# Kernel optimization log

Measured on AMD Instinct MI355X. Metric: run time of the kernel, lower is better.

Reference implementation:

```python
import jax, jax.numpy as jnp
import numpy as np

B = 1024
IN_Q = 2048
IN_KV = 2048
NH = 16
D = 64
INNER = NH * D
TF = 4
NC = 2
EPS = 1e-5
SLOPE = 0.01  # LeakyReLU default negative slope


def setup_inputs() -> dict:
    key = jax.random.key(0)
    ks = jax.random.split(key, 8)
    s = 0.02
    return {
        "q_input": jax.random.normal(ks[0], (B, IN_Q), jnp.float32),
        "kv_input": jax.random.normal(ks[1], (B, IN_KV), jnp.float32),
        "Wq": jax.random.normal(ks[2], (INNER, IN_Q), jnp.float32) * s,
        "bq": jax.random.normal(ks[3], (INNER,), jnp.float32) * s,
        "Wkv": jax.random.normal(ks[4], (2 * INNER, IN_KV), jnp.float32) * s,
        "bkv": jax.random.normal(ks[5], (2 * INNER,), jnp.float32) * s,
        "bn_w": jnp.ones((TF,), jnp.float32),
        "bn_b": jnp.zeros((TF,), jnp.float32),
        "Wo": jax.random.normal(ks[6], (NC, TF), jnp.float32) * s,
        "bo": jax.random.normal(ks[7], (NC,), jnp.float32) * s,
    }


def reference(q_input, kv_input, Wq, bq, Wkv, bkv, bn_w, bn_b, Wo, bo):
    b = q_input.shape[0]
    # projections: [B, NH, D] and [B, NH, 2D]
    q = (q_input @ Wq.T + bq).reshape(b, NH, D)
    kv = (kv_input @ Wkv.T + bkv).reshape(b, NH, 2 * D)
    k, v = kv[..., :D], kv[..., D:]
    # sim[b,n] = k[b,n,:] . q[b,n,:]  (per-head scalar score)
    sim = jnp.einsum("bnd,bnd->bn", k, q)
    att = jax.nn.softmax(sim, axis=-1)  # softmax over heads
    # torch.matmul([B,NH], [B,NH,D]) broadcast -> out[i,j,:] = sum_n att[j,n] v[i,n,:]
    att_out = jnp.einsum("jn,ind->ijd", att, v)  # [B, B, D]
    flat = att_out.reshape(b, b * D)  # [B, B*D]
    # AdaptiveAvgPool1d to TF bins (L % TF == 0 -> exact reshape-mean)
    pooled = flat.reshape(b, TF, (b * D) // TF).mean(axis=-1)  # [B, TF]
    x = jnp.where(pooled >= 0, pooled, SLOPE * pooled)  # LeakyReLU
    # BatchNorm1d, train mode (batch stats, biased variance)
    mean = x.mean(axis=0)
    var = x.var(axis=0)
    x = (x - mean) * jax.lax.rsqrt(var + EPS) * bn_w + bn_b
    # dropout(p=0.0) is identity
    return x @ Wo.T + bo  # [B, NC]
```

## Files before the change

### kernel.cpp

```cpp
#include <hip/hip_runtime.h>
#include <hip/hip_bf16.h>

#define EPS 1e-5f
#define SLOPE 0.01f

typedef __attribute__((ext_vector_type(8))) short bfrag8;
typedef __attribute__((ext_vector_type(4))) float f32x4;

#define AS1 __attribute__((address_space(1)))
#define AS3 __attribute__((address_space(3)))

#define WS_SIM_OFF   0u
#define WS_S_OFF     65536u
#define WS_WVS_OFF   131072u
#define WS_BVS_OFF   262144u
#define WS_OUT_OFF   262208u
#define WS_AIMG_OFF  8650816u
#define WS_BIMG_OFF  25428032u

__device__ __forceinline__ unsigned short f2bf(float f) {
    union { float f; unsigned int u; } x; x.f = f;
    unsigned int r = (x.u + 0x7FFFu + ((x.u >> 16) & 1u)) >> 16;
    return (unsigned short)r;
}
__device__ __forceinline__ uint4 pack8(const float4& a, const float4& b) {
    uint4 r;
    r.x = (unsigned)f2bf(a.x) | ((unsigned)f2bf(a.y) << 16);
    r.y = (unsigned)f2bf(a.z) | ((unsigned)f2bf(a.w) << 16);
    r.z = (unsigned)f2bf(b.x) | ((unsigned)f2bf(b.y) << 16);
    r.w = (unsigned)f2bf(b.z) | ((unsigned)f2bf(b.w) << 16);
    return r;
}

#define PREP_A    524288
#define PREP_B2   (PREP_A + 524288)
#define PREP_WVSE (PREP_B2 + 32768)
#define PREP_END  (PREP_WVSE + 16)

__global__ __launch_bounds__(256) void prep_kernel(
        const float* __restrict__ qin, const float* __restrict__ kvin,
        const float* __restrict__ Wq, const float* __restrict__ Wkv,
        const float* __restrict__ bkv, unsigned char* __restrict__ ws) {
    int gid = blockIdx.x * 256 + threadIdx.x;
    if (gid < PREP_A) {
        int p  = gid & 511;
        int kt = (gid >> 9) & 31;
        int mt = (gid >> 14) & 15;
        int s2 = gid >> 18;
        int rit = p >> 3;
        int gk = (p & 7) ^ (rit & 7);
        int row = mt * 64 + rit;
        int k = kt * 64 + gk * 8;
        const float* src = (s2 ? kvin : qin) + (size_t)row * 2048 + k;
        float4 v0 = *(const float4*)src;
        float4 v1 = *(const float4*)(src + 4);
        *(uint4*)(ws + WS_AIMG_OFF + (size_t)gid * 16) = pack8(v0, v1);
    } else if (gid < PREP_B2) {
        int g2 = gid - PREP_A;
        int p  = g2 & 511;
        int kt = (g2 >> 9) & 31;
        int nt = g2 >> 14;
        int cit = p >> 3;
        int gk = (p & 7) ^ (cit & 7);
        int col = nt * 64 + cit;
        int k = kt * 64 + gk * 8;
        const float* wrow;
        if (col < 1024) wrow = Wq + (size_t)col * 2048;
        else {
            int c2 = col - 1024;
            wrow = Wkv + (size_t)(((c2 >> 6) << 7) + (c2 & 63)) * 2048;
        }
        float4 v0 = *(const float4*)(wrow + k);
        float4 v1 = *(const float4*)(wrow + k + 4);
        *(uint4*)(ws + WS_BIMG_OFF + (size_t)g2 * 16) = pack8(v0, v1);
    } else if (gid < PREP_WVSE) {
        int g2 = gid - PREP_B2;
        int n = g2 >> 11, c = g2 & 2047;
        const float* base = Wkv + (size_t)(n * 128 + 64) * 2048 + c;
        float s = 0.f;
        #pragma unroll 8
        for (int d = 0; d < 64; ++d) s += base[(size_t)d * 2048];
        ((float*)(ws + WS_WVS_OFF))[c * 16 + n] = s;
    } else if (gid < PREP_END) {
        int n = gid - PREP_WVSE;
        float b = 0.f;
        #pragma unroll
        for (int d = 0; d < 64; ++d) b += bkv[n * 128 + 64 + d];
        ((float*)(ws + WS_BVS_OFF))[n] = b;
    }
}

__global__ __launch_bounds__(256, 2) void gemm_qk_kernel(unsigned char* __restrict__ ws) {
    __shared__ alignas(16) unsigned short LA[3][4096];
    __shared__ alignas(16) unsigned short LB[3][4096];

    const int t = threadIdx.x;
    const int w = t >> 6, l = t & 63;
    const int nt = blockIdx.x, mt = blockIdx.y;
    const int wr = w >> 1, wc = w & 1;
    const int lrow = l & 15, lhi = l >> 4;

    const unsigned char* aBase = ws + WS_AIMG_OFF
        + (size_t)((nt >= 16) ? 4194304u : 0u) + (size_t)mt * 262144u;
    const unsigned char* bBase = ws + WS_BIMG_OFF + (size_t)nt * 262144u;
    float* Out = (float*)(ws + WS_OUT_OFF);

    int offA[2][2], offB[2][2];
    #pragma unroll
    for (int ks = 0; ks < 2; ++ks)
        #pragma unroll
        for (int i = 0; i < 2; ++i) {
            int rA = wr * 32 + i * 16 + lrow;
            int rB = wc * 32 + i * 16 + lrow;
            offA[ks][i] = rA * 128 + (((ks * 4 + lhi) ^ (rA & 7)) << 4);
            offB[ks][i] = rB * 128 + (((ks * 4 + lhi) ^ (rB & 7)) << 4);
        }

    f32x4 acc00 = (f32x4)0.f, acc01 = (f32x4)0.f, acc10 = (f32x4)0.f, acc11 = (f32x4)0.f;

#define STAGE(kt_, buf_) do {                                                        \
    const unsigned char* _as = aBase + (size_t)(kt_) * 8192;                         \
    const unsigned char* _bs = bBase + (size_t)(kt_) * 8192;                         \
    unsigned char* _ad = ((unsigned char*)&LA[0][0]) + (size_t)(buf_) * 8192;        \
    unsigned char* _bd = ((unsigned char*)&LB[0][0]) + (size_t)(buf_) * 8192;        \
    _Pragma("unroll")                                                                \
    for (int _j = 0; _j < 2; ++_j) {                                                 \
        int _p = _j * 256 + t;                                                       \
        __builtin_amdgcn_global_load_lds(                                            \
            (const AS1 unsigned int*)(const void*)(_as + _p * 16),                   \
            (AS3 unsigned int*)(void*)(_ad + _p * 16), 16, 0, 0);                    \
        __builtin_amdgcn_global_load_lds(                                            \
            (const AS1 unsigned int*)(const void*)(_bs + _p * 16),                   \
            (AS3 unsigned int*)(void*)(_bd + _p * 16), 16, 0, 0);                    \
    } } while (0)

    STAGE(0, 0);
    STAGE(1, 1);
    asm volatile("s_waitcnt vmcnt(4)" ::: "memory");
    __builtin_amdgcn_sched_barrier(0);
    __builtin_amdgcn_s_barrier();
    __builtin_amdgcn_sched_barrier(0);

    int cur = 0, nxt = 2;
    for (int kt = 0; kt < 32; ++kt) {
        const char* la = (const char*)&LA[0][0] + cur * 8192;
        const char* lb = (const char*)&LB[0][0] + cur * 8192;
        bfrag8 fa00 = *(const bfrag8*)(la + offA[0][0]);
        bfrag8 fa01 = *(const bfrag8*)(la + offA[0][1]);
        bfrag8 fa10 = *(const bfrag8*)(la + offA[1][0]);
        bfrag8 fa11 = *(const bfrag8*)(la + offA[1][1]);
        bfrag8 fb00 = *(const bfrag8*)(lb + offB[0][0]);
        bfrag8 fb01 = *(const bfrag8*)(lb + offB[0][1]);
        bfrag8 fb10 = *(const bfrag8*)(lb + offB[1][0]);
        bfrag8 fb11 = *(const bfrag8*)(lb + offB[1][1]);
        acc00 = __builtin_amdgcn_mfma_f32_16x16x32_bf16(fa00, fb00, acc00, 0, 0, 0);
        acc01 = __builtin_amdgcn_mfma_f32_16x16x32_bf16(fa00, fb01, acc01, 0, 0, 0);
        acc10 = __builtin_amdgcn_mfma_f32_16x16x32_bf16(fa01, fb00, acc10, 0, 0, 0);
        acc11 = __builtin_amdgcn_mfma_f32_16x16x32_bf16(fa01, fb01, acc11, 0, 0, 0);
        acc00 = __builtin_amdgcn_mfma_f32_16x16x32_bf16(fa10, fb10, acc00, 0, 0, 0);
        acc01 = __builtin_amdgcn_mfma_f32_16x16x32_bf16(fa10, fb11, acc01, 0, 0, 0);
        acc10 = __builtin_amdgcn_mfma_f32_16x16x32_bf16(fa11, fb10, acc10, 0, 0, 0);
        acc11 = __builtin_amdgcn_mfma_f32_16x16x32_bf16(fa11, fb11, acc11, 0, 0, 0);
        if (kt < 30) {
            STAGE(kt + 2, nxt);
            asm volatile("s_waitcnt vmcnt(4)" ::: "memory");
        } else {
            asm volatile("s_waitcnt vmcnt(0)" ::: "memory");
        }
        __builtin_amdgcn_sched_barrier(0);
        __builtin_amdgcn_s_barrier();
        __builtin_amdgcn_sched_barrier(0);
        cur = (cur == 2) ? 0 : cur + 1;
        nxt = (nxt == 2) ? 0 : nxt + 1;
    }
#undef STAGE

    f32x4 acc[2][2] = {{acc00, acc01}, {acc10, acc11}};
    #pragma unroll
    for (int mi = 0; mi < 2; ++mi)
        #pragma unroll
        for (int ni = 0; ni < 2; ++ni) {
            int col = nt * 64 + wc * 32 + ni * 16 + lrow;
            #pragma unroll
            for (int r = 0; r < 4; ++r) {
                int row = mt * 64 + wr * 32 + mi * 16 + lhi * 4 + r;
                Out[(size_t)row * 2048 + col] = acc[mi][ni][r];
            }
        }
}

__global__ __launch_bounds__(256) void sim_s_kernel(
        const float* __restrict__ bq, const float* __restrict__ bkv,
        const float* __restrict__ kvin, unsigned char* __restrict__ ws) {
    int b = blockIdx.x, t = threadIdx.x;
    int w = t >> 6, l = t & 63;
    {
        const float* orow = (const float*)(ws + WS_OUT_OFF) + (size_t)b * 2048;
        float* sim = (float*)(ws + WS_SIM_OFF);
        #pragma unroll
        for (int hh = 0; hh < 4; ++hh) {
            int h = w * 4 + hh;
            float qv = orow[h * 64 + l]        + bq[h * 64 + l];
            float kv = orow[1024 + h * 64 + l] + bkv[h * 128 + l];
            float p = qv * kv;
            p += __shfl_xor(p, 1);  p += __shfl_xor(p, 2);
            p += __shfl_xor(p, 4);  p += __shfl_xor(p, 8);
            p += __shfl_xor(p, 16); p += __shfl_xor(p, 32);
            if (l == 0) sim[b * 16 + h] = p;
        }
    }
    __shared__ float SW[4][16];
    int n = t & 15, g = t >> 4;
    const float* kvrow = kvin + (size_t)b * 2048;
    const float* wv = (const float*)(ws + WS_WVS_OFF);
    float p = 0.f;
    #pragma unroll 4
    for (int tt = 0; tt < 128; ++tt) {
        int c = g + (tt << 4);
        p = fmaf(kvrow[c], wv[c * 16 + n], p);
    }
    p += __shfl_xor(p, 16);
    p += __shfl_xor(p, 32);
    if (l < 16) SW[w][n] = p;
    __syncthreads();
    if (t < 16) {
        float sv = SW[0][t] + SW[1][t] + SW[2][t] + SW[3][t]
                 + ((const float*)(ws + WS_BVS_OFF))[t];
        ((float*)(ws + WS_S_OFF))[b * 16 + t] = sv;
    }
}

__global__ __launch_bounds__(1024) void final_kernel(
        const float* __restrict__ bn_w, const float* __restrict__ bn_b,
        const float* __restrict__ Wo, const float* __restrict__ bo,
        const unsigned char* __restrict__ ws, float* __restrict__ out) {
    int t = threadIdx.x;
    int w = t >> 6;
    int l = t & 63;
    __shared__ float Aw[16][16];
    __shared__ float Af[4][16];
    __shared__ float SWs[16][8];
    __shared__ float FS[8];
    __shared__ float sc[4], sh[4];

    float a16[16];
    {
        const float* srow = (const float*)(ws + WS_SIM_OFF) + (size_t)t * 16;
        float4 v0 = *(const float4*)(srow + 0);
        float4 v1 = *(const float4*)(srow + 4);
        float4 v2 = *(const float4*)(srow + 8);
        float4 v3 = *(const float4*)(srow + 12);
        a16[0]=v0.x; a16[1]=v0.y; a16[2]=v0.z; a16[3]=v0.w;
        a16[4]=v1.x; a16[5]=v1.y; a16[6]=v1.z; a16[7]=v1.w;
        a16[8]=v2.x; a16[9]=v2.y; a16[10]=v2.z; a16[11]=v2.w;
        a16[12]=v3.x; a16[13]=v3.y; a16[14]=v3.z; a16[15]=v3.w;
        float m = a16[0];
        #pragma unroll
        for (int n = 1; n < 16; ++n) m = fmaxf(m, a16[n]);
        float den = 0.f;
        #pragma unroll
        for (int n = 0; n < 16; ++n) { a16[n] = expf(a16[n] - m); den += a16[n]; }
        float inv = 1.f / den;
        #pragma unroll
        for (int n = 0; n < 16; ++n) a16[n] *= inv;
    }
    #pragma unroll
    for (int n = 0; n < 16; ++n) {
        float p = a16[n];
        p += __shfl_xor(p, 1);  p += __shfl_xor(p, 2);
        p += __shfl_xor(p, 4);  p += __shfl_xor(p, 8);
        p += __shfl_xor(p, 16); p += __shfl_xor(p, 32);
        a16[n] = p;
    }
    if (l == 0) {
        #pragma unroll
        for (int n = 0; n < 16; ++n) Aw[w][n] = a16[n];
    }
    __syncthreads();
    if (t < 64) {
        int f = t >> 4, n = t & 15;
        Af[f][n] = Aw[4*f][n] + Aw[4*f+1][n] + Aw[4*f+2][n] + Aw[4*f+3][n];
    }
    __syncthreads();

    float sv[16];
    {
        const float* srow = (const float*)(ws + WS_S_OFF) + (size_t)t * 16;
        float4 v0 = *(const float4*)(srow + 0);
        float4 v1 = *(const float4*)(srow + 4);
        float4 v2 = *(const float4*)(srow + 8);
        float4 v3 = *(const float4*)(srow + 12);
        sv[0]=v0.x; sv[1]=v0.y; sv[2]=v0.z; sv[3]=v0.w;
        sv[4]=v1.x; sv[5]=v1.y; sv[6]=v1.z; sv[7]=v1.w;
        sv[8]=v2.x; sv[9]=v2.y; sv[10]=v2.z; sv[11]=v2.w;
        sv[12]=v3.x; sv[13]=v3.y; sv[14]=v3.z; sv[15]=v3.w;
    }
    float x[4];
    #pragma unroll
    for (int f = 0; f < 4; ++f) {
        float p = 0.f;
        #pragma unroll
        for (int n = 0; n < 16; ++n) p = fmaf(Af[f][n], sv[n], p);
        p *= (1.f / 16384.f);
        x[f] = (p >= 0.f) ? p : SLOPE * p;
    }

    float st[8];
    #pragma unroll
    for (int f = 0; f < 4; ++f) { st[f] = x[f]; st[4 + f] = x[f] * x[f]; }
    #pragma unroll
    for (int j = 0; j < 8; ++j) {
        float p = st[j];
        p += __shfl_xor(p, 1);  p += __shfl_xor(p, 2);
        p += __shfl_xor(p, 4);  p += __shfl_xor(p, 8);
        p += __shfl_xor(p, 16); p += __shfl_xor(p, 32);
        st[j] = p;
    }
    if (l == 0) {
        #pragma unroll
        for (int j = 0; j < 8; ++j) SWs[w][j] = st[j];
    }
    __syncthreads();
    if (t < 8) {
        float p = 0.f;
        #pragma unroll
        for (int ww = 0; ww < 16; ++ww) p += SWs[ww][t];
        FS[t] = p;
    }
    __syncthreads();
    if (t < 4) {
        float mean = FS[t] * (1.f / 1024.f);
        float var  = FS[4 + t] * (1.f / 1024.f) - mean * mean;
        float s = bn_w[t] / sqrtf(var + EPS);
        sc[t] = s;
        sh[t] = bn_b[t] - mean * s;
    }
    __syncthreads();

    float o0 = bo[0], o1 = bo[1];
    #pragma unroll
    for (int f = 0; f < 4; ++f) {
        float xh = x[f] * sc[f] + sh[f];
        o0 = fmaf(xh, Wo[f], o0);
        o1 = fmaf(xh, Wo[4 + f], o1);
    }
    *(float2*)(out + (size_t)t * 2) = make_float2(o0, o1);
}

extern "C" void kernel_launch(void* const* d_in, const int* in_sizes, int n_in,
                              void* d_out, int out_size, void* d_ws, size_t ws_size,
                              hipStream_t stream) {
    const float* q_input  = (const float*)d_in[0];
    const float* kv_input = (const float*)d_in[1];
    const float* Wq   = (const float*)d_in[2];
    const float* bq   = (const float*)d_in[3];
    const float* Wkv  = (const float*)d_in[4];
    const float* bkv  = (const float*)d_in[5];
    const float* bn_w = (const float*)d_in[6];
    const float* bn_b = (const float*)d_in[7];
    const float* Wo   = (const float*)d_in[8];
    const float* bo   = (const float*)d_in[9];
    float* out = (float*)d_out;
    unsigned char* ws = (unsigned char*)d_ws;

    hipLaunchKernelGGL(prep_kernel, dim3((PREP_END + 255) / 256), dim3(256), 0, stream,
                       q_input, kv_input, Wq, Wkv, bkv, ws);
    hipLaunchKernelGGL(gemm_qk_kernel, dim3(32, 16), dim3(256), 0, stream, ws);
    hipLaunchKernelGGL(sim_s_kernel, dim3(1024), dim3(256), 0, stream,
                       bq, bkv, kv_input, ws);
    hipLaunchKernelGGL(final_kernel, dim3(1), dim3(1024), 0, stream,
                       bn_w, bn_b, Wo, bo, ws, out);
}
```

Measured before the change: 62.94 us.

## Enlarge GEMM tiles to 128x128 with split-K over two partial outputs

The projection GEMM moves from 64x64 tiles and 512 blocks to 128x128 tiles split along K into two halves, giving 256 blocks. Each writes a partial result to its own buffer, and the sim kernel adds the two partials. The prep layout changes to match the larger tiles, and the pipeline becomes four-stage with 16 accumulators per wave. The aim is better operand reuse per LDS load and fewer global loads, at the cost of extra partial-sum traffic, 128KB of LDS per block and lower occupancy.

New measurement: 66.25 us. 5.3% more time.

```diff
diff --git a/kernel.cpp b/kernel.cpp
--- a/kernel.cpp
+++ b/kernel.cpp
@@ -14,8 +14,9 @@
 #define WS_S_OFF     65536u
 #define WS_WVS_OFF   131072u
 #define WS_BVS_OFF   262144u
-#define WS_OUT_OFF   262208u
-#define WS_AIMG_OFF  8650816u
+#define WS_OUT0_OFF  262208u
+#define WS_OUT1_OFF  8650816u
+#define WS_AIMG_OFF  17039424u
 #define WS_BIMG_OFF  25428032u
 
 __device__ __forceinline__ unsigned short f2bf(float f) {
@@ -43,27 +44,27 @@
         const float* __restrict__ bkv, unsigned char* __restrict__ ws) {
     int gid = blockIdx.x * 256 + threadIdx.x;
     if (gid < PREP_A) {
-        int p  = gid & 511;
-        int kt = (gid >> 9) & 31;
-        int mt = (gid >> 14) & 15;
-        int s2 = gid >> 18;
+        int p   = gid & 1023;
+        int ktg = (gid >> 10) & 31;
+        int mt  = (gid >> 15) & 7;
+        int s2  = gid >> 18;
         int rit = p >> 3;
-        int gk = (p & 7) ^ (rit & 7);
-        int row = mt * 64 + rit;
-        int k = kt * 64 + gk * 8;
+        int gk  = (p & 7) ^ (rit & 7);
+        int row = mt * 128 + rit;
+        int k   = ktg * 64 + gk * 8;
         const float* src = (s2 ? kvin : qin) + (size_t)row * 2048 + k;
         float4 v0 = *(const float4*)src;
         float4 v1 = *(const float4*)(src + 4);
         *(uint4*)(ws + WS_AIMG_OFF + (size_t)gid * 16) = pack8(v0, v1);
     } else if (gid < PREP_B2) {
-        int g2 = gid - PREP_A;
-        int p  = g2 & 511;
-        int kt = (g2 >> 9) & 31;
-        int nt = g2 >> 14;
+        int g2  = gid - PREP_A;
+        int p   = g2 & 1023;
+        int ktg = (g2 >> 10) & 31;
+        int nt  = g2 >> 15;
         int cit = p >> 3;
-        int gk = (p & 7) ^ (cit & 7);
-        int col = nt * 64 + cit;
-        int k = kt * 64 + gk * 8;
+        int gk  = (p & 7) ^ (cit & 7);
+        int col = nt * 128 + cit;
+        int k   = ktg * 64 + gk * 8;
         const float* wrow;
         if (col < 1024) wrow = Wq + (size_t)col * 2048;
         else {
@@ -90,41 +91,47 @@
     }
 }
 
-__global__ __launch_bounds__(256, 2) void gemm_qk_kernel(unsigned char* __restrict__ ws) {
-    __shared__ alignas(16) unsigned short LA[3][4096];
-    __shared__ alignas(16) unsigned short LB[3][4096];
+__global__ __launch_bounds__(256) void gemm_qk_kernel(unsigned char* __restrict__ ws) {
+    __shared__ alignas(16) unsigned short LA[4][8192];
+    __shared__ alignas(16) unsigned short LB[4][8192];
 
     const int t = threadIdx.x;
     const int w = t >> 6, l = t & 63;
-    const int nt = blockIdx.x, mt = blockIdx.y;
+    const int nt = blockIdx.x, mt = blockIdx.y, kz = blockIdx.z;
     const int wr = w >> 1, wc = w & 1;
     const int lrow = l & 15, lhi = l >> 4;
 
     const unsigned char* aBase = ws + WS_AIMG_OFF
-        + (size_t)((nt >= 16) ? 4194304u : 0u) + (size_t)mt * 262144u;
-    const unsigned char* bBase = ws + WS_BIMG_OFF + (size_t)nt * 262144u;
-    float* Out = (float*)(ws + WS_OUT_OFF);
-
-    int offA[2][2], offB[2][2];
+        + (size_t)((nt >= 8) ? 4194304u : 0u) + (size_t)mt * 524288u
+        + (size_t)kz * 262144u;
+    const unsigned char* bBase = ws + WS_BIMG_OFF
+        + (size_t)nt * 524288u + (size_t)kz * 262144u;
+    float* Out = (float*)(ws + (kz ? WS_OUT1_OFF : WS_OUT0_OFF));
+
+    int offA[2][4], offB[2][4];
     #pragma unroll
     for (int ks = 0; ks < 2; ++ks)
         #pragma unroll
-        for (int i = 0; i < 2; ++i) {
-            int rA = wr * 32 + i * 16 + lrow;
-            int rB = wc * 32 + i * 16 + lrow;
+        for (int i = 0; i < 4; ++i) {
+            int rA = wr * 64 + i * 16 + lrow;
+            int rB = wc * 64 + i * 16 + lrow;
             offA[ks][i] = rA * 128 + (((ks * 4 + lhi) ^ (rA & 7)) << 4);
             offB[ks][i] = rB * 128 + (((ks * 4 + lhi) ^ (rB & 7)) << 4);
         }
 
-    f32x4 acc00 = (f32x4)0.f, acc01 = (f32x4)0.f, acc10 = (f32x4)0.f, acc11 = (f32x4)0.f;
+    f32x4 acc[4][4];
+    #pragma unroll
+    for (int mi = 0; mi < 4; ++mi)
+        #pragma unroll
+        for (int ni = 0; ni < 4; ++ni) acc[mi][ni] = (f32x4)0.f;
 
 #define STAGE(kt_, buf_) do {                                                        \
-    const unsigned char* _as = aBase + (size_t)(kt_) * 8192;                         \
-    const unsigned char* _bs = bBase + (size_t)(kt_) * 8192;                         \
-    unsigned char* _ad = ((unsigned char*)&LA[0][0]) + (size_t)(buf_) * 8192;        \
-    unsigned char* _bd = ((unsigned char*)&LB[0][0]) + (size_t)(buf_) * 8192;        \
+    const unsigned char* _as = aBase + (size_t)(kt_) * 16384;                        \
+    const unsigned char* _bs = bBase + (size_t)(kt_) * 16384;                        \
+    unsigned char* _ad = ((unsigned char*)&LA[0][0]) + (size_t)(buf_) * 16384;       \
+    unsigned char* _bd = ((unsigned char*)&LB[0][0]) + (size_t)(buf_) * 16384;       \
     _Pragma("unroll")                                                                \
-    for (int _j = 0; _j < 2; ++_j) {                                                 \
+    for (int _j = 0; _j < 4; ++_j) {                                                 \
         int _p = _j * 256 + t;                                                       \
         __builtin_amdgcn_global_load_lds(                                            \
             (const AS1 unsigned int*)(const void*)(_as + _p * 16),                   \
@@ -136,54 +143,49 @@
 
     STAGE(0, 0);
     STAGE(1, 1);
-    asm volatile("s_waitcnt vmcnt(4)" ::: "memory");
+    STAGE(2, 2);
+    asm volatile("s_waitcnt vmcnt(16)" ::: "memory");
     __builtin_amdgcn_sched_barrier(0);
     __builtin_amdgcn_s_barrier();
     __builtin_amdgcn_sched_barrier(0);
 
-    int cur = 0, nxt = 2;
-    for (int kt = 0; kt < 32; ++kt) {
-        const char* la = (const char*)&LA[0][0] + cur * 8192;
-        const char* lb = (const char*)&LB[0][0] + cur * 8192;
-        bfrag8 fa00 = *(const bfrag8*)(la + offA[0][0]);
-        bfrag8 fa01 = *(const bfrag8*)(la + offA[0][1]);
-        bfrag8 fa10 = *(const bfrag8*)(la + offA[1][0]);
-        bfrag8 fa11 = *(const bfrag8*)(la + offA[1][1]);
-        bfrag8 fb00 = *(const bfrag8*)(lb + offB[0][0]);
-        bfrag8 fb01 = *(const bfrag8*)(lb + offB[0][1]);
-        bfrag8 fb10 = *(const bfrag8*)(lb + offB[1][0]);
-        bfrag8 fb11 = *(const bfrag8*)(lb + offB[1][1]);
-        acc00 = __builtin_amdgcn_mfma_f32_16x16x32_bf16(fa00, fb00, acc00, 0, 0, 0);
-        acc01 = __builtin_amdgcn_mfma_f32_16x16x32_bf16(fa00, fb01, acc01, 0, 0, 0);
-        acc10 = __builtin_amdgcn_mfma_f32_16x16x32_bf16(fa01, fb00, acc10, 0, 0, 0);
-        acc11 = __builtin_amdgcn_mfma_f32_16x16x32_bf16(fa01, fb01, acc11, 0, 0, 0);
-        acc00 = __builtin_amdgcn_mfma_f32_16x16x32_bf16(fa10, fb10, acc00, 0, 0, 0);
-        acc01 = __builtin_amdgcn_mfma_f32_16x16x32_bf16(fa10, fb11, acc01, 0, 0, 0);
-        acc10 = __builtin_amdgcn_mfma_f32_16x16x32_bf16(fa11, fb10, acc10, 0, 0, 0);
-        acc11 = __builtin_amdgcn_mfma_f32_16x16x32_bf16(fa11, fb11, acc11, 0, 0, 0);
-        if (kt < 30) {
-            STAGE(kt + 2, nxt);
-            asm volatile("s_waitcnt vmcnt(4)" ::: "memory");
-        } else {
-            asm volatile("s_waitcnt vmcnt(0)" ::: "memory");
-        }
+    for (int kt = 0; kt < 16; ++kt) {
+        const int cur = kt & 3;
+        if (kt <= 12) STAGE(kt + 3, (kt + 3) & 3);
+        const char* la = (const char*)&LA[0][0] + (size_t)cur * 16384;
+        const char* lb = (const char*)&LB[0][0] + (size_t)cur * 16384;
+        #pragma unroll
+        for (int ks = 0; ks < 2; ++ks) {
+            bfrag8 fa[4], fb[4];
+            #pragma unroll
+            for (int i = 0; i < 4; ++i) {
+                fa[i] = *(const bfrag8*)(la + offA[ks][i]);
+                fb[i] = *(const bfrag8*)(lb + offB[ks][i]);
+            }
+            #pragma unroll
+            for (int mi = 0; mi < 4; ++mi)
+                #pragma unroll
+                for (int ni = 0; ni < 4; ++ni)
+                    acc[mi][ni] = __builtin_amdgcn_mfma_f32_16x16x32_bf16(
+                        fa[mi], fb[ni], acc[mi][ni], 0, 0, 0);
+        }
+        if (kt <= 12)      asm volatile("s_waitcnt vmcnt(16)" ::: "memory");
+        else if (kt == 13) asm volatile("s_waitcnt vmcnt(8)"  ::: "memory");
+        else               asm volatile("s_waitcnt vmcnt(0)"  ::: "memory");
         __builtin_amdgcn_sched_barrier(0);
         __builtin_amdgcn_s_barrier();
         __builtin_amdgcn_sched_barrier(0);
-        cur = (cur == 2) ? 0 : cur + 1;
-        nxt = (nxt == 2) ? 0 : nxt + 1;
     }
 #undef STAGE
 
-    f32x4 acc[2][2] = {{acc00, acc01}, {acc10, acc11}};
-    #pragma unroll
-    for (int mi = 0; mi < 2; ++mi)
-        #pragma unroll
-        for (int ni = 0; ni < 2; ++ni) {
-            int col = nt * 64 + wc * 32 + ni * 16 + lrow;
+    #pragma unroll
+    for (int mi = 0; mi < 4; ++mi)
+        #pragma unroll
+        for (int ni = 0; ni < 4; ++ni) {
+            int col = nt * 128 + wc * 64 + ni * 16 + lrow;
             #pragma unroll
             for (int r = 0; r < 4; ++r) {
-                int row = mt * 64 + wr * 32 + mi * 16 + lhi * 4 + r;
+                int row = mt * 128 + wr * 64 + mi * 16 + lhi * 4 + r;
                 Out[(size_t)row * 2048 + col] = acc[mi][ni][r];
             }
         }
@@ -195,13 +197,14 @@
     int b = blockIdx.x, t = threadIdx.x;
     int w = t >> 6, l = t & 63;
     {
-        const float* orow = (const float*)(ws + WS_OUT_OFF) + (size_t)b * 2048;
+        const float* o0 = (const float*)(ws + WS_OUT0_OFF) + (size_t)b * 2048;
+        const float* o1 = (const float*)(ws + WS_OUT1_OFF) + (size_t)b * 2048;
         float* sim = (float*)(ws + WS_SIM_OFF);
         #pragma unroll
         for (int hh = 0; hh < 4; ++hh) {
             int h = w * 4 + hh;
-            float qv = orow[h * 64 + l]        + bq[h * 64 + l];
-            float kv = orow[1024 + h * 64 + l] + bkv[h * 128 + l];
+            float qv = o0[h * 64 + l]        + o1[h * 64 + l]        + bq[h * 64 + l];
+            float kv = o0[1024 + h * 64 + l] + o1[1024 + h * 64 + l] + bkv[h * 128 + l];
             float p = qv * kv;
             p += __shfl_xor(p, 1);  p += __shfl_xor(p, 2);
             p += __shfl_xor(p, 4);  p += __shfl_xor(p, 8);
@@ -365,7 +368,7 @@
 
     hipLaunchKernelGGL(prep_kernel, dim3((PREP_END + 255) / 256), dim3(256), 0, stream,
                        q_input, kv_input, Wq, Wkv, bkv, ws);
-    hipLaunchKernelGGL(gemm_qk_kernel, dim3(32, 16), dim3(256), 0, stream, ws);
+    hipLaunchKernelGGL(gemm_qk_kernel, dim3(16, 8, 2), dim3(256), 0, stream, ws);
     hipLaunchKernelGGL(sim_s_kernel, dim3(1024), dim3(256), 0, stream,
                        bq, bkv, kv_input, ws);
     hipLaunchKernelGGL(final_kernel, dim3(1), dim3(1024), 0, stream,
```

## Convert activations to bf16 inside GEMM and read B fragments directly from global

Applied to the files above, without the earlier changes.

The prep kernel no longer pre-converts q/kv activations into a swizzled bf16 image. The GEMM now loads fp32 activations, converts them in registers with v_cvt_pk_bf16_f32, and writes them to a double-buffered LDS tile. Weights are pre-packed in MFMA fragment order so each wave reads its B fragments straight from global memory without LDS staging. This removes a full round trip of the activation image through memory and halves LDS use, at the cost of register-staged loads and uncached-in-LDS B reads whose latency may be less hidden.

Result: slower. 68.86 us (+9.4%).

```diff
diff --git a/kernel.cpp b/kernel.cpp
--- a/kernel.cpp
+++ b/kernel.cpp
@@ -6,17 +6,13 @@
 
 typedef __attribute__((ext_vector_type(8))) short bfrag8;
 typedef __attribute__((ext_vector_type(4))) float f32x4;
-
-#define AS1 __attribute__((address_space(1)))
-#define AS3 __attribute__((address_space(3)))
 
 #define WS_SIM_OFF   0u
 #define WS_S_OFF     65536u
 #define WS_WVS_OFF   131072u
 #define WS_BVS_OFF   262144u
 #define WS_OUT_OFF   262208u
-#define WS_AIMG_OFF  8650816u
-#define WS_BIMG_OFF  25428032u
+#define WS_BIMG_OFF  8650816u
 
 __device__ __forceinline__ unsigned short f2bf(float f) {
     union { float f; unsigned int u; } x; x.f = f;
@@ -31,39 +27,29 @@
     r.w = (unsigned)f2bf(b.z) | ((unsigned)f2bf(b.w) << 16);
     return r;
 }
-
-#define PREP_A    524288
-#define PREP_B2   (PREP_A + 524288)
+__device__ __forceinline__ unsigned cvtpk(float lo, float hi) {
+    unsigned r;
+    asm("v_cvt_pk_bf16_f32 %0, %1, %2" : "=v"(r) : "v"(lo), "v"(hi));
+    return r;
+}
+
+#define PREP_B2   524288
 #define PREP_WVSE (PREP_B2 + 32768)
 #define PREP_END  (PREP_WVSE + 16)
 
 __global__ __launch_bounds__(256) void prep_kernel(
-        const float* __restrict__ qin, const float* __restrict__ kvin,
         const float* __restrict__ Wq, const float* __restrict__ Wkv,
         const float* __restrict__ bkv, unsigned char* __restrict__ ws) {
     int gid = blockIdx.x * 256 + threadIdx.x;
-    if (gid < PREP_A) {
-        int p  = gid & 511;
-        int kt = (gid >> 9) & 31;
-        int mt = (gid >> 14) & 15;
-        int s2 = gid >> 18;
-        int rit = p >> 3;
-        int gk = (p & 7) ^ (rit & 7);
-        int row = mt * 64 + rit;
-        int k = kt * 64 + gk * 8;
-        const float* src = (s2 ? kvin : qin) + (size_t)row * 2048 + k;
-        float4 v0 = *(const float4*)src;
-        float4 v1 = *(const float4*)(src + 4);
-        *(uint4*)(ws + WS_AIMG_OFF + (size_t)gid * 16) = pack8(v0, v1);
-    } else if (gid < PREP_B2) {
-        int g2 = gid - PREP_A;
-        int p  = g2 & 511;
-        int kt = (g2 >> 9) & 31;
-        int nt = g2 >> 14;
-        int cit = p >> 3;
-        int gk = (p & 7) ^ (cit & 7);
-        int col = nt * 64 + cit;
-        int k = kt * 64 + gk * 8;
+    if (gid < PREP_B2) {
+        int l   = gid & 63;
+        int ni  = (gid >> 6) & 1;
+        int ks  = (gid >> 7) & 1;
+        int kt  = (gid >> 8) & 31;
+        int wcg = (gid >> 13) & 1;
+        int nt  = gid >> 14;
+        int col = nt * 64 + wcg * 32 + ni * 16 + (l & 15);
+        int k   = kt * 64 + ks * 32 + (l >> 4) * 8;
         const float* wrow;
         if (col < 1024) wrow = Wq + (size_t)col * 2048;
         else {
@@ -72,7 +58,7 @@
         }
         float4 v0 = *(const float4*)(wrow + k);
         float4 v1 = *(const float4*)(wrow + k + 4);
-        *(uint4*)(ws + WS_BIMG_OFF + (size_t)g2 * 16) = pack8(v0, v1);
+        *(uint4*)(ws + WS_BIMG_OFF + (size_t)gid * 16) = pack8(v0, v1);
     } else if (gid < PREP_WVSE) {
         int g2 = gid - PREP_B2;
         int n = g2 >> 11, c = g2 & 2047;
@@ -90,90 +76,101 @@
     }
 }
 
-__global__ __launch_bounds__(256, 2) void gemm_qk_kernel(unsigned char* __restrict__ ws) {
-    __shared__ alignas(16) unsigned short LA[3][4096];
-    __shared__ alignas(16) unsigned short LB[3][4096];
+__global__ __launch_bounds__(256) void gemm_qk_kernel(
+        const float* __restrict__ qin, const float* __restrict__ kvin,
+        unsigned char* __restrict__ ws) {
+    __shared__ alignas(16) unsigned short LA[2][4096];
 
     const int t = threadIdx.x;
     const int w = t >> 6, l = t & 63;
     const int nt = blockIdx.x, mt = blockIdx.y;
     const int wr = w >> 1, wc = w & 1;
     const int lrow = l & 15, lhi = l >> 4;
-
-    const unsigned char* aBase = ws + WS_AIMG_OFF
-        + (size_t)((nt >= 16) ? 4194304u : 0u) + (size_t)mt * 262144u;
-    const unsigned char* bBase = ws + WS_BIMG_OFF + (size_t)nt * 262144u;
+    const int m0 = mt * 64;
+
+    const int arow = t >> 2, aq4 = t & 3;
+    const int gk0 = aq4 * 2, gk1 = gk0 + 1;
+    const float* aSrc = ((nt >= 16) ? kvin : qin) + (size_t)(m0 + arow) * 2048;
+    const int adst0 = arow * 128 + ((gk0 ^ (arow & 7)) << 4);
+    const int adst1 = arow * 128 + ((gk1 ^ (arow & 7)) << 4);
+    unsigned char* lds = (unsigned char*)&LA[0][0];
+
+    const unsigned char* bP = ws + WS_BIMG_OFF
+        + (size_t)(nt * 2 + wc) * 131072 + (size_t)l * 16;
+
     float* Out = (float*)(ws + WS_OUT_OFF);
 
-    int offA[2][2], offB[2][2];
+    int offA[2][2];
     #pragma unroll
     for (int ks = 0; ks < 2; ++ks)
         #pragma unroll
         for (int i = 0; i < 2; ++i) {
-            int rA = wr * 32 + i * 16 + lrow;
-            int rB = wc * 32 + i * 16 + lrow;
-            offA[ks][i] = rA * 128 + (((ks * 4 + lhi) ^ (rA & 7)) << 4);
-            offB[ks][i] = rB * 128 + (((ks * 4 + lhi) ^ (rB & 7)) << 4);
+            int r = wr * 32 + i * 16 + lrow;
+            offA[ks][i] = r * 128 + (((ks * 4 + lhi) ^ (r & 7)) << 4);
         }
 
     f32x4 acc00 = (f32x4)0.f, acc01 = (f32x4)0.f, acc10 = (f32x4)0.f, acc11 = (f32x4)0.f;
 
-#define STAGE(kt_, buf_) do {                                                        \
-    const unsigned char* _as = aBase + (size_t)(kt_) * 8192;                         \
-    const unsigned char* _bs = bBase + (size_t)(kt_) * 8192;                         \
-    unsigned char* _ad = ((unsigned char*)&LA[0][0]) + (size_t)(buf_) * 8192;        \
-    unsigned char* _bd = ((unsigned char*)&LB[0][0]) + (size_t)(buf_) * 8192;        \
-    _Pragma("unroll")                                                                \
-    for (int _j = 0; _j < 2; ++_j) {                                                 \
-        int _p = _j * 256 + t;                                                       \
-        __builtin_amdgcn_global_load_lds(                                            \
-            (const AS1 unsigned int*)(const void*)(_as + _p * 16),                   \
-            (AS3 unsigned int*)(void*)(_ad + _p * 16), 16, 0, 0);                    \
-        __builtin_amdgcn_global_load_lds(                                            \
-            (const AS1 unsigned int*)(const void*)(_bs + _p * 16),                   \
-            (AS3 unsigned int*)(void*)(_bd + _p * 16), 16, 0, 0);                    \
+#define LOAD_A(kt_, S) do {                                                   \
+    S[0] = *(const float4*)(aSrc + (kt_) * 64 + gk0 * 8);                     \
+    S[1] = *(const float4*)(aSrc + (kt_) * 64 + gk0 * 8 + 4);                 \
+    S[2] = *(const float4*)(aSrc + (kt_) * 64 + gk1 * 8);                     \
+    S[3] = *(const float4*)(aSrc + (kt_) * 64 + gk1 * 8 + 4); } while (0)
+
+#define WRITE_A(S, buf_) do {                                                 \
+    uint4 _u0, _u1;                                                           \
+    _u0.x = cvtpk(S[0].x, S[0].y); _u0.y = cvtpk(S[0].z, S[0].w);             \
+    _u0.z = cvtpk(S[1].x, S[1].y); _u0.w = cvtpk(S[1].z, S[1].w);             \
+    _u1.x = cvtpk(S[2].x, S[2].y); _u1.y = cvtpk(S[2].z, S[2].w);             \
+    _u1.z = cvtpk(S[3].x, S[3].y); _u1.w = cvtpk(S[3].z, S[3].w);             \
+    *(uint4*)(lds + (buf_) * 8192 + adst0) = _u0;                             \
+    *(uint4*)(lds + (buf_) * 8192 + adst1) = _u1; } while (0)
+
+#define BARRIER() do {                                                        \
+    asm volatile("s_waitcnt lgkmcnt(0)" ::: "memory");                        \
+    __builtin_amdgcn_sched_barrier(0);                                        \
+    __builtin_amdgcn_s_barrier();                                             \
+    __builtin_amdgcn_sched_barrier(0); } while (0)
+
+#define COMPUTE(kt_, buf_) do {                                               \
+    const char* _la = (const char*)lds + (buf_) * 8192;                       \
+    const unsigned char* _bp = bP + (size_t)(kt_) * 4096;                     \
+    _Pragma("unroll")                                                         \
+    for (int _ks = 0; _ks < 2; ++_ks) {                                       \
+        bfrag8 _fa0 = *(const bfrag8*)(_la + offA[_ks][0]);                   \
+        bfrag8 _fa1 = *(const bfrag8*)(_la + offA[_ks][1]);                   \
+        bfrag8 _fb0 = *(const bfrag8*)(_bp + _ks * 2048);                     \
+        bfrag8 _fb1 = *(const bfrag8*)(_bp + _ks * 2048 + 1024);              \
+        acc00 = __builtin_amdgcn_mfma_f32_16x16x32_bf16(_fa0, _fb0, acc00, 0, 0, 0); \
+        acc01 = __builtin_amdgcn_mfma_f32_16x16x32_bf16(_fa0, _fb1, acc01, 0, 0, 0); \
+        acc10 = __builtin_amdgcn_mfma_f32_16x16x32_bf16(_fa1, _fb0, acc10, 0, 0, 0); \
+        acc11 = __builtin_amdgcn_mfma_f32_16x16x32_bf16(_fa1, _fb1, acc11, 0, 0, 0); \
     } } while (0)
 
-    STAGE(0, 0);
-    STAGE(1, 1);
-    asm volatile("s_waitcnt vmcnt(4)" ::: "memory");
-    __builtin_amdgcn_sched_barrier(0);
-    __builtin_amdgcn_s_barrier();
-    __builtin_amdgcn_sched_barrier(0);
-
-    int cur = 0, nxt = 2;
-    for (int kt = 0; kt < 32; ++kt) {
-        const char* la = (const char*)&LA[0][0] + cur * 8192;
-        const char* lb = (const char*)&LB[0][0] + cur * 8192;
-        bfrag8 fa00 = *(const bfrag8*)(la + offA[0][0]);
-        bfrag8 fa01 = *(const bfrag8*)(la + offA[0][1]);
-        bfrag8 fa10 = *(const bfrag8*)(la + offA[1][0]);
-        bfrag8 fa11 = *(const bfrag8*)(la + offA[1][1]);
-        bfrag8 fb00 = *(const bfrag8*)(lb + offB[0][0]);
-        bfrag8 fb01 = *(const bfrag8*)(lb + offB[0][1]);
-        bfrag8 fb10 = *(const bfrag8*)(lb + offB[1][0]);
-        bfrag8 fb11 = *(const bfrag8*)(lb + offB[1][1]);
-        acc00 = __builtin_amdgcn_mfma_f32_16x16x32_bf16(fa00, fb00, acc00, 0, 0, 0);
-        acc01 = __builtin_amdgcn_mfma_f32_16x16x32_bf16(fa00, fb01, acc01, 0, 0, 0);
-        acc10 = __builtin_amdgcn_mfma_f32_16x16x32_bf16(fa01, fb00, acc10, 0, 0, 0);
-        acc11 = __builtin_amdgcn_mfma_f32_16x16x32_bf16(fa01, fb01, acc11, 0, 0, 0);
-        acc00 = __builtin_amdgcn_mfma_f32_16x16x32_bf16(fa10, fb10, acc00, 0, 0, 0);
-        acc01 = __builtin_amdgcn_mfma_f32_16x16x32_bf16(fa10, fb11, acc01, 0, 0, 0);
-        acc10 = __builtin_amdgcn_mfma_f32_16x16x32_bf16(fa11, fb10, acc10, 0, 0, 0);
-        acc11 = __builtin_amdgcn_mfma_f32_16x16x32_bf16(fa11, fb11, acc11, 0, 0, 0);
-        if (kt < 30) {
-            STAGE(kt + 2, nxt);
-            asm volatile("s_waitcnt vmcnt(4)" ::: "memory");
-        } else {
-            asm volatile("s_waitcnt vmcnt(0)" ::: "memory");
-        }
-        __builtin_amdgcn_sched_barrier(0);
-        __builtin_amdgcn_s_barrier();
-        __builtin_amdgcn_sched_barrier(0);
-        cur = (cur == 2) ? 0 : cur + 1;
-        nxt = (nxt == 2) ? 0 : nxt + 1;
-    }
-#undef STAGE
+    float4 E[4], O[4];
+
+    LOAD_A(0, E);
+    WRITE_A(E, 0);
+    LOAD_A(1, O);
+    BARRIER();
+
+    for (int j = 0; j < 16; ++j) {
+        const int kt = 2 * j;
+        if (j < 15) LOAD_A(kt + 2, E);
+        COMPUTE(kt, 0);
+        WRITE_A(O, 1);
+        BARRIER();
+        if (j < 15) LOAD_A(kt + 3, O);
+        COMPUTE(kt + 1, 1);
+        if (j < 15) {
+            WRITE_A(E, 0);
+            BARRIER();
+        }
+    }
+#undef LOAD_A
+#undef WRITE_A
+#undef BARRIER
+#undef COMPUTE
 
     f32x4 acc[2][2] = {{acc00, acc01}, {acc10, acc11}};
     #pragma unroll
@@ -183,7 +180,7 @@
             int col = nt * 64 + wc * 32 + ni * 16 + lrow;
             #pragma unroll
             for (int r = 0; r < 4; ++r) {
-                int row = mt * 64 + wr * 32 + mi * 16 + lhi * 4 + r;
+                int row = m0 + wr * 32 + mi * 16 + lhi * 4 + r;
                 Out[(size_t)row * 2048 + col] = acc[mi][ni][r];
             }
         }
@@ -364,8 +361,9 @@
     unsigned char* ws = (unsigned char*)d_ws;
 
     hipLaunchKernelGGL(prep_kernel, dim3((PREP_END + 255) / 256), dim3(256), 0, stream,
-                       q_input, kv_input, Wq, Wkv, bkv, ws);
-    hipLaunchKernelGGL(gemm_qk_kernel, dim3(32, 16), dim3(256), 0, stream, ws);
+                       Wq, Wkv, bkv, ws);
+    hipLaunchKernelGGL(gemm_qk_kernel, dim3(32, 16), dim3(256), 0, stream,
+                       q_input, kv_input, ws);
     hipLaunchKernelGGL(sim_s_kernel, dim3(1024), dim3(256), 0, stream,
                        bq, bkv, kv_input, ws);
     hipLaunchKernelGGL(final_kernel, dim3(1), dim3(1024), 0, stream,
```

## Fuse per-head q·k score into projection GEMM epilogue with atomic accumulation

Applied to the files above, without the earlier changes.

Reorganizes the B-weight image so each GEMM block computes matching 32-column halves of the Q and K projections for one head. The q and k tiles are combined in the epilogue via shared memory, reduced with shuffles, and atomically added into the sim buffer, which prep now zeroes. This removes the 8 MB fp32 projection output write and its re-read in the follow-up kernel. In exchange each block loads three A/B tiles per k-step instead of two, uses more LDS, and the sim values are summed with float atomics, so their order is nondeterministic.

New measurement: 60.56 us. 1.04x faster.

```diff
diff --git a/kernel.cpp b/kernel.cpp
--- a/kernel.cpp
+++ b/kernel.cpp
@@ -14,9 +14,8 @@
 #define WS_S_OFF     65536u
 #define WS_WVS_OFF   131072u
 #define WS_BVS_OFF   262144u
-#define WS_OUT_OFF   262208u
-#define WS_AIMG_OFF  8650816u
-#define WS_BIMG_OFF  25428032u
+#define WS_AIMG_OFF  262208u
+#define WS_BIMG_OFF  8650816u
 
 __device__ __forceinline__ unsigned short f2bf(float f) {
     union { float f; unsigned int u; } x; x.f = f;
@@ -35,7 +34,8 @@
 #define PREP_A    524288
 #define PREP_B2   (PREP_A + 524288)
 #define PREP_WVSE (PREP_B2 + 32768)
-#define PREP_END  (PREP_WVSE + 16)
+#define PREP_SIMZ (PREP_WVSE + 16384)
+#define PREP_END  (PREP_SIMZ + 16)
 
 __global__ __launch_bounds__(256) void prep_kernel(
         const float* __restrict__ qin, const float* __restrict__ kvin,
@@ -59,17 +59,14 @@
         int g2 = gid - PREP_A;
         int p  = g2 & 511;
         int kt = (g2 >> 9) & 31;
-        int nt = g2 >> 14;
+        int dh = (g2 >> 14) & 1;
+        int h  = g2 >> 15;
         int cit = p >> 3;
         int gk = (p & 7) ^ (cit & 7);
-        int col = nt * 64 + cit;
         int k = kt * 64 + gk * 8;
         const float* wrow;
-        if (col < 1024) wrow = Wq + (size_t)col * 2048;
-        else {
-            int c2 = col - 1024;
-            wrow = Wkv + (size_t)(((c2 >> 6) << 7) + (c2 & 63)) * 2048;
-        }
+        if (cit < 32) wrow = Wq  + (size_t)(h * 64 + dh * 32 + cit) * 2048;
+        else          wrow = Wkv + (size_t)(h * 128 + dh * 32 + (cit - 32)) * 2048;
         float4 v0 = *(const float4*)(wrow + k);
         float4 v1 = *(const float4*)(wrow + k + 4);
         *(uint4*)(ws + WS_BIMG_OFF + (size_t)g2 * 16) = pack8(v0, v1);
@@ -81,8 +78,10 @@
         #pragma unroll 8
         for (int d = 0; d < 64; ++d) s += base[(size_t)d * 2048];
         ((float*)(ws + WS_WVS_OFF))[c * 16 + n] = s;
+    } else if (gid < PREP_SIMZ) {
+        ((float*)(ws + WS_SIM_OFF))[gid - PREP_WVSE] = 0.f;
     } else if (gid < PREP_END) {
-        int n = gid - PREP_WVSE;
+        int n = gid - PREP_SIMZ;
         float b = 0.f;
         #pragma unroll
         for (int d = 0; d < 64; ++d) b += bkv[n * 128 + 64 + d];
@@ -90,80 +89,86 @@
     }
 }
 
-__global__ __launch_bounds__(256, 2) void gemm_qk_kernel(unsigned char* __restrict__ ws) {
-    __shared__ alignas(16) unsigned short LA[3][4096];
+__global__ __launch_bounds__(256, 2) void gemm_sim_kernel(unsigned char* __restrict__ ws,
+        const float* __restrict__ bq, const float* __restrict__ bkv) {
+    __shared__ alignas(16) unsigned short LAq[3][4096];
+    __shared__ alignas(16) unsigned short LAkv[3][4096];
     __shared__ alignas(16) unsigned short LB[3][4096];
 
     const int t = threadIdx.x;
     const int w = t >> 6, l = t & 63;
-    const int nt = blockIdx.x, mt = blockIdx.y;
-    const int wr = w >> 1, wc = w & 1;
+    const int hd = blockIdx.x, mt = blockIdx.y;
+    const int h = hd >> 1, dh = hd & 1;
+    const int qk = w >> 1, wr = w & 1;
     const int lrow = l & 15, lhi = l >> 4;
-
-    const unsigned char* aBase = ws + WS_AIMG_OFF
-        + (size_t)((nt >= 16) ? 4194304u : 0u) + (size_t)mt * 262144u;
-    const unsigned char* bBase = ws + WS_BIMG_OFF + (size_t)nt * 262144u;
-    float* Out = (float*)(ws + WS_OUT_OFF);
+    const int m0 = mt * 64;
+
+    const unsigned char* aqBase = ws + WS_AIMG_OFF + (size_t)mt * 262144u;
+    const unsigned char* akBase = aqBase + 4194304u;
+    const unsigned char* bBase  = ws + WS_BIMG_OFF + (size_t)hd * 262144u;
+    float* sim = (float*)(ws + WS_SIM_OFF);
 
     int offA[2][2], offB[2][2];
     #pragma unroll
     for (int ks = 0; ks < 2; ++ks)
         #pragma unroll
         for (int i = 0; i < 2; ++i) {
-            int rA = wr * 32 + i * 16 + lrow;
-            int rB = wc * 32 + i * 16 + lrow;
-            offA[ks][i] = rA * 128 + (((ks * 4 + lhi) ^ (rA & 7)) << 4);
-            offB[ks][i] = rB * 128 + (((ks * 4 + lhi) ^ (rB & 7)) << 4);
+            int r = wr * 32 + i * 16 + lrow;
+            int c = qk * 32 + i * 16 + lrow;
+            offA[ks][i] = r * 128 + (((ks * 4 + lhi) ^ (r & 7)) << 4);
+            offB[ks][i] = c * 128 + (((ks * 4 + lhi) ^ (c & 7)) << 4);
         }
 
     f32x4 acc00 = (f32x4)0.f, acc01 = (f32x4)0.f, acc10 = (f32x4)0.f, acc11 = (f32x4)0.f;
 
 #define STAGE(kt_, buf_) do {                                                        \
-    const unsigned char* _as = aBase + (size_t)(kt_) * 8192;                         \
-    const unsigned char* _bs = bBase + (size_t)(kt_) * 8192;                         \
-    unsigned char* _ad = ((unsigned char*)&LA[0][0]) + (size_t)(buf_) * 8192;        \
-    unsigned char* _bd = ((unsigned char*)&LB[0][0]) + (size_t)(buf_) * 8192;        \
+    const unsigned char* _aq = aqBase + (size_t)(kt_) * 8192;                        \
+    const unsigned char* _ak = akBase + (size_t)(kt_) * 8192;                        \
+    const unsigned char* _b  = bBase  + (size_t)(kt_) * 8192;                        \
+    unsigned char* _dq = ((unsigned char*)&LAq[0][0])  + (size_t)(buf_) * 8192;      \
+    unsigned char* _dk = ((unsigned char*)&LAkv[0][0]) + (size_t)(buf_) * 8192;      \
+    unsigned char* _db = ((unsigned char*)&LB[0][0])   + (size_t)(buf_) * 8192;      \
     _Pragma("unroll")                                                                \
     for (int _j = 0; _j < 2; ++_j) {                                                 \
         int _p = _j * 256 + t;                                                       \
         __builtin_amdgcn_global_load_lds(                                            \
-            (const AS1 unsigned int*)(const void*)(_as + _p * 16),                   \
-            (AS3 unsigned int*)(void*)(_ad + _p * 16), 16, 0, 0);                    \
+            (const AS1 unsigned int*)(const void*)(_aq + _p * 16),                   \
+            (AS3 unsigned int*)(void*)(_dq + _p * 16), 16, 0, 0);                    \
         __builtin_amdgcn_global_load_lds(                                            \
-            (const AS1 unsigned int*)(const void*)(_bs + _p * 16),                   \
-            (AS3 unsigned int*)(void*)(_bd + _p * 16), 16, 0, 0);                    \
+            (const AS1 unsigned int*)(const void*)(_ak + _p * 16),                   \
+            (AS3 unsigned int*)(void*)(_dk + _p * 16), 16, 0, 0);                    \
+        __builtin_amdgcn_global_load_lds(                                            \
+            (const AS1 unsigned int*)(const void*)(_b + _p * 16),                    \
+            (AS3 unsigned int*)(void*)(_db + _p * 16), 16, 0, 0);                    \
     } } while (0)
 
     STAGE(0, 0);
     STAGE(1, 1);
-    asm volatile("s_waitcnt vmcnt(4)" ::: "memory");
+    asm volatile("s_waitcnt vmcnt(6)" ::: "memory");
     __builtin_amdgcn_sched_barrier(0);
     __builtin_amdgcn_s_barrier();
     __builtin_amdgcn_sched_barrier(0);
 
     int cur = 0, nxt = 2;
     for (int kt = 0; kt < 32; ++kt) {
-        const char* la = (const char*)&LA[0][0] + cur * 8192;
-        const char* lb = (const char*)&LB[0][0] + cur * 8192;
-        bfrag8 fa00 = *(const bfrag8*)(la + offA[0][0]);
-        bfrag8 fa01 = *(const bfrag8*)(la + offA[0][1]);
-        bfrag8 fa10 = *(const bfrag8*)(la + offA[1][0]);
-        bfrag8 fa11 = *(const bfrag8*)(la + offA[1][1]);
-        bfrag8 fb00 = *(const bfrag8*)(lb + offB[0][0]);
-        bfrag8 fb01 = *(const bfrag8*)(lb + offB[0][1]);
-        bfrag8 fb10 = *(const bfrag8*)(lb + offB[1][0]);
-        bfrag8 fb11 = *(const bfrag8*)(lb + offB[1][1]);
-        acc00 = __builtin_amdgcn_mfma_f32_16x16x32_bf16(fa00, fb00, acc00, 0, 0, 0);
-        acc01 = __builtin_amdgcn_mfma_f32_16x16x32_bf16(fa00, fb01, acc01, 0, 0, 0);
-        acc10 = __builtin_amdgcn_mfma_f32_16x16x32_bf16(fa01, fb00, acc10, 0, 0, 0);
-        acc11 = __builtin_amdgcn_mfma_f32_16x16x32_bf16(fa01, fb01, acc11, 0, 0, 0);
-        acc00 = __builtin_amdgcn_mfma_f32_16x16x32_bf16(fa10, fb10, acc00, 0, 0, 0);
-        acc01 = __builtin_amdgcn_mfma_f32_16x16x32_bf16(fa10, fb11, acc01, 0, 0, 0);
-        acc10 = __builtin_amdgcn_mfma_f32_16x16x32_bf16(fa11, fb10, acc10, 0, 0, 0);
-        acc11 = __builtin_amdgcn_mfma_f32_16x16x32_bf16(fa11, fb11, acc11, 0, 0, 0);
+        {
+            const char* Ab = (const char*)(qk ? &LAkv[0][0] : &LAq[0][0]) + cur * 8192;
+            const char* Bb = (const char*)&LB[0][0] + cur * 8192;
+            #pragma unroll
+            for (int ks = 0; ks < 2; ++ks) {
+                bfrag8 fa0 = *(const bfrag8*)(Ab + offA[ks][0]);
+                bfrag8 fa1 = *(const bfrag8*)(Ab + offA[ks][1]);
+                bfrag8 fb0 = *(const bfrag8*)(Bb + offB[ks][0]);
+                bfrag8 fb1 = *(const bfrag8*)(Bb + offB[ks][1]);
+                acc00 = __builtin_amdgcn_mfma_f32_16x16x32_bf16(fa0, fb0, acc00, 0, 0, 0);
+                acc01 = __builtin_amdgcn_mfma_f32_16x16x32_bf16(fa0, fb1, acc01, 0, 0, 0);
+                acc10 = __builtin_amdgcn_mfma_f32_16x16x32_bf16(fa1, fb0, acc10, 0, 0, 0);
+                acc11 = __builtin_amdgcn_mfma_f32_16x16x32_bf16(fa1, fb1, acc11, 0, 0, 0);
+            }
+        }
         if (kt < 30) {
             STAGE(kt + 2, nxt);
-            asm volatile("s_waitcnt vmcnt(4)" ::: "memory");
+            asm volatile("s_waitcnt vmcnt(6)" ::: "memory");
         } else {
             asm volatile("s_waitcnt vmcnt(0)" ::: "memory");
         }
@@ -176,39 +181,59 @@
 #undef STAGE
 
     f32x4 acc[2][2] = {{acc00, acc01}, {acc10, acc11}};
+    float biasv[2];
+    #pragma unroll
+    for (int ni = 0; ni < 2; ++ni) {
+        int d = dh * 32 + ni * 16 + lrow;
+        biasv[ni] = qk ? bkv[h * 128 + d] : bq[h * 64 + d];
+    }
     #pragma unroll
     for (int mi = 0; mi < 2; ++mi)
         #pragma unroll
-        for (int ni = 0; ni < 2; ++ni) {
-            int col = nt * 64 + wc * 32 + ni * 16 + lrow;
+        for (int ni = 0; ni < 2; ++ni)
+            #pragma unroll
+            for (int r = 0; r < 4; ++r)
+                acc[mi][ni][r] += biasv[ni];
+
+    float (*Cq)[32] = (float(*)[32])&LAq[0][0];
+    if (!qk) {
+        #pragma unroll
+        for (int mi = 0; mi < 2; ++mi)
+            #pragma unroll
+            for (int ni = 0; ni < 2; ++ni)
+                #pragma unroll
+                for (int r = 0; r < 4; ++r)
+                    Cq[wr * 32 + mi * 16 + lhi * 4 + r][ni * 16 + lrow] = acc[mi][ni][r];
+    }
+    __syncthreads();
+    if (qk) {
+        #pragma unroll
+        for (int mi = 0; mi < 2; ++mi) {
+            float pv[4];
             #pragma unroll
             for (int r = 0; r < 4; ++r) {
-                int row = mt * 64 + wr * 32 + mi * 16 + lhi * 4 + r;
-                Out[(size_t)row * 2048 + col] = acc[mi][ni][r];
+                int row = wr * 32 + mi * 16 + lhi * 4 + r;
+                pv[r] = Cq[row][lrow]      * acc[mi][0][r]
+                      + Cq[row][16 + lrow] * acc[mi][1][r];
+            }
+            #pragma unroll
+            for (int r = 0; r < 4; ++r) {
+                float v = pv[r];
+                v += __shfl_xor(v, 1); v += __shfl_xor(v, 2);
+                v += __shfl_xor(v, 4); v += __shfl_xor(v, 8);
+                if ((l & 15) == 0) {
+                    int row = wr * 32 + mi * 16 + (l >> 4) * 4 + r;
+                    atomicAdd(&sim[(m0 + row) * 16 + h], v);
+                }
             }
         }
-}
-
-__global__ __launch_bounds__(256) void sim_s_kernel(
-        const float* __restrict__ bq, const float* __restrict__ bkv,
+    }
+}
+
+__global__ __launch_bounds__(256) void s_kernel(
         const float* __restrict__ kvin, unsigned char* __restrict__ ws) {
     int b = blockIdx.x, t = threadIdx.x;
     int w = t >> 6, l = t & 63;
-    {
-        const float* orow = (const float*)(ws + WS_OUT_OFF) + (size_t)b * 2048;
-        float* sim = (float*)(ws + WS_SIM_OFF);
-        #pragma unroll
-        for (int hh = 0; hh < 4; ++hh) {
-            int h = w * 4 + hh;
-            float qv = orow[h * 64 + l]        + bq[h * 64 + l];
-            float kv = orow[1024 + h * 64 + l] + bkv[h * 128 + l];
-            float p = qv * kv;
-            p += __shfl_xor(p, 1);  p += __shfl_xor(p, 2);
-            p += __shfl_xor(p, 4);  p += __shfl_xor(p, 8);
-            p += __shfl_xor(p, 16); p += __shfl_xor(p, 32);
-            if (l == 0) sim[b * 16 + h] = p;
-        }
-    }
     __shared__ float SW[4][16];
     int n = t & 15, g = t >> 4;
     const float* kvrow = kvin + (size_t)b * 2048;
@@ -365,9 +390,9 @@
 
     hipLaunchKernelGGL(prep_kernel, dim3((PREP_END + 255) / 256), dim3(256), 0, stream,
                        q_input, kv_input, Wq, Wkv, bkv, ws);
-    hipLaunchKernelGGL(gemm_qk_kernel, dim3(32, 16), dim3(256), 0, stream, ws);
-    hipLaunchKernelGGL(sim_s_kernel, dim3(1024), dim3(256), 0, stream,
-                       bq, bkv, kv_input, ws);
+    hipLaunchKernelGGL(gemm_sim_kernel, dim3(32, 16), dim3(256), 0, stream,
+                       ws, bq, bkv);
+    hipLaunchKernelGGL(s_kernel, dim3(1024), dim3(256), 0, stream, kv_input, ws);
     hipLaunchKernelGGL(final_kernel, dim3(1), dim3(1024), 0, stream,
                        bn_w, bn_b, Wo, bo, ws, out);
 }
```
